# Kernel tuning notes

Measured on AMD Instinct MI355X. Metric: run time of the kernel, lower is better.

## Reference

```python
import jax, jax.numpy as jnp
import numpy as np

E, H, O = 300, 256, 2            # embedding_size, hidden_size, output_size
N_SENT, SENT_LEN, CLAIM_LEN = 2048, 64, 64


def setup_inputs() -> dict:
    key = jax.random.key(0)
    ks = jax.random.split(key, 24)
    rn = lambda k, shape, s=0.05: (jax.random.normal(k, shape, jnp.float32) * s)
    return {
        "claim": jax.random.normal(ks[0], (CLAIM_LEN, E), jnp.float32),
        "sentences": jax.random.normal(ks[1], (N_SENT, SENT_LEN, E), jnp.float32),
        # claim GRU (PyTorch layout: W_ih (3H,E), W_hh (3H,H), gates ordered r,z,n)
        "Wih_c": rn(ks[2], (3 * H, E)), "Whh_c": rn(ks[3], (3 * H, H)),
        "bih_c": rn(ks[4], (3 * H,)), "bhh_c": rn(ks[5], (3 * H,)),
        # sentence GRU
        "Wih_s": rn(ks[6], (3 * H, E)), "Whh_s": rn(ks[7], (3 * H, H)),
        "bih_s": rn(ks[8], (3 * H,)), "bhh_s": rn(ks[9], (3 * H,)),
        # gates (no bias)
        "Wg_s": rn(ks[10], (1, H)), "Wg_c": rn(ks[11], (1, H)),
        # coherence attention
        "Wac": rn(ks[12], (H, H)), "bac": rn(ks[13], (H,)),
        "Was": rn(ks[14], (1, H)), "bas": rn(ks[15], (1,)),
        # extension linear (H, 2H)
        "Wext": rn(ks[16], (H, 2 * H)), "bext": rn(ks[17], (H,)),
        # joint linear (H, 4H), no bias
        "Wj": rn(ks[18], (H, 4 * H)),
        # entailment attention
        "Wae": rn(ks[19], (1, H)), "bae": rn(ks[20], (1,)),
        # final classifier
        "Wf": rn(ks[21], (O, H)), "bf": rn(ks[22], (O,)),
    }


def _gru_last(x, Wih, Whh, bih, bhh):
    """x: (T, B, E) -> final hidden state (B, H). PyTorch GRU math, zero init."""
    B = x.shape[1]
    Hd = Whh.shape[1]
    gi = jnp.einsum('tbe,ge->tbg', x, Wih) + bih  # (T, B, 3H), input projections

    def step(h, gi_t):
        gh = h @ Whh.T + bhh
        ir, iz, inn = jnp.split(gi_t, 3, axis=-1)
        hr, hz, hn = jnp.split(gh, 3, axis=-1)
        r = jax.nn.sigmoid(ir + hr)
        z = jax.nn.sigmoid(iz + hz)
        n = jnp.tanh(inn + r * hn)
        return (1.0 - z) * n + z * h, None

    h0 = jnp.zeros((B, Hd), x.dtype)
    hT, _ = jax.lax.scan(step, h0, gi)
    return hT


def reference(claim, sentences, Wih_c, Whh_c, bih_c, bhh_c,
              Wih_s, Whh_s, bih_s, bhh_s, Wg_s, Wg_c,
              Wac, bac, Was, bas, Wext, bext, Wj, Wae, bae, Wf, bf):
    # claim encoder: (T,1,E) -> hc (1,H)
    hc = _gru_last(claim[:, None, :], Wih_c, Whh_c, bih_c, bhh_c)
    # batched sentence encoder (replaces the per-sentence Python loop)
    HS = _gru_last(jnp.transpose(sentences, (1, 0, 2)), Wih_s, Whh_s, bih_s, bhh_s)  # (N,H)
    # gated fusion of sentence reps with claim rep
    g = jax.nn.sigmoid(HS @ Wg_s.T + hc @ Wg_c.T)          # (N,1)
    HSg = g * HS + (1.0 - g) * hc                           # (N,H)
    # coherence attention over sentences (row-wise softmax)
    scores = (HSg @ Wac.T + bac) @ HSg.T + (HSg @ Was.T + bas)  # (N,N)
    coh = jax.nn.softmax(scores, axis=1)
    H_apo = coh @ HSg                                       # (N,H)
    H_tilde = jnp.tanh(jnp.concatenate([HS, H_apo], axis=1) @ Wext.T + bext)  # (N,H)
    # joint claim-sentence entailment features (replaces per-row loop)
    hc_b = jnp.broadcast_to(hc, H_tilde.shape)
    joint_in = jnp.concatenate(
        [hc_b, H_tilde, hc * H_tilde, jnp.abs(hc - H_tilde)], axis=1)  # (N,4H)
    H_c_s = jnp.tanh(joint_in @ Wj.T)                       # (N,H)
    # entailment attention (softmax over sentence axis)
    ae = jnp.tanh(H_c_s @ Wae.T + bae)                      # (N,1)
    w = jax.nn.softmax(ae, axis=0)                          # (N,1)
    h_c_S = w.T @ H_c_s                                     # (1,H)
    return jax.nn.sigmoid(h_c_S @ Wf.T + bf)                # (1,O)
```

## Files before the change

kernel.cpp:

```cpp
#include <hip/hip_runtime.h>

typedef unsigned short u16;
typedef unsigned int u32;
typedef short bf16x8 __attribute__((ext_vector_type(8)));
typedef float f32x4 __attribute__((ext_vector_type(4)));
typedef u16 u16x4v __attribute__((ext_vector_type(4)));

__device__ __forceinline__ float b2f(u16 h){ return __uint_as_float(((unsigned)h)<<16); }
__device__ __forceinline__ u16 f2b(float f){
  unsigned u = __float_as_uint(f);
  u += 0x7fffu + ((u>>16)&1u);
  return (u16)(u>>16);
}
__device__ __forceinline__ float sigm(float x){ return 1.f/(1.f+__expf(-x)); }
__device__ __forceinline__ float tanh_(float x){
  float ax=fabsf(x), e=__expf(-2.f*ax), t=(1.f-e)/(1.f+e);
  return x<0.f? -t : t;
}
__device__ __forceinline__ bf16x8 ld8a(const u16* p){
  union{ u16x4v h[2]; bf16x8 v; } u;
  u.h[0]=*(const u16x4v*)p; u.h[1]=*(const u16x4v*)(p+4); return u.v;
}
__device__ __forceinline__ f32x4 mfma16(bf16x8 a, bf16x8 b, f32x4 c){
  return __builtin_amdgcn_mfma_f32_16x16x32_bf16(a,b,c,0,0,0);
}

__global__ __launch_bounds__(256) void cvt_kernel(
    const float* __restrict__ WihS, const float* __restrict__ WhhS,
    const float* __restrict__ WihC, const float* __restrict__ WhhC,
    const float* __restrict__ Wac,  const float* __restrict__ Wext,
    const float* __restrict__ Wj,
    const float* __restrict__ bihS, const float* __restrict__ bhhS,
    const float* __restrict__ bihC, const float* __restrict__ bhhC,
    u16* __restrict__ WihP, u16* __restrict__ WhhSb,
    u16* __restrict__ WihCP, u16* __restrict__ WhhCb,
    u16* __restrict__ WacB, u16* __restrict__ WextB, u16* __restrict__ WjB,
    float* __restrict__ biasGI, float* __restrict__ biasGIC)
{
  const int seg = blockIdx.y;
  int n;
  switch(seg){
    case 0: n = 768*320; break;  case 1: n = 196608; break;
    case 2: n = 768*320; break;  case 3: n = 196608; break;
    case 4: n = 65536; break;    case 5: n = 131072; break;
    case 6: n = 262144; break;   default: n = 1536; break;
  }
  for (int i = blockIdx.x*256 + threadIdx.x; i < n; i += gridDim.x*256){
    switch(seg){
      case 0: { int r=i/320, c=i-r*320; WihP[i]  = (c<300)? f2b(WihS[r*300+c]) : (u16)0; } break;
      case 1: WhhSb[i] = f2b(WhhS[i]); break;
      case 2: { int r=i/320, c=i-r*320; WihCP[i] = (c<300)? f2b(WihC[r*300+c]) : (u16)0; } break;
      case 3: WhhCb[i] = f2b(WhhC[i]); break;
      case 4: WacB[i]  = f2b(Wac[i]);  break;
      case 5: WextB[i] = f2b(Wext[i]); break;
      case 6: WjB[i]   = f2b(Wj[i]);   break;
      default:
        if (i < 768) biasGI[i] = bihS[i] + (i < 512 ? bhhS[i] : 0.f);
        else { int j = i - 768; biasGIC[j] = bihC[j] + (j < 512 ? bhhC[j] : 0.f); }
        break;
    }
  }
}

__global__ __launch_bounds__(512) void gi_kernel(
    const int pass,
    const float* __restrict__ sents, const float* __restrict__ claim,
    const u16* __restrict__ WihP, const float* __restrict__ biasGI,
    const u16* __restrict__ WihCP, const float* __restrict__ biasGIC,
    u16* __restrict__ gi_b, float* __restrict__ giC)
{
  __shared__ __align__(16) u16 SA[64*320];
  const int tid=threadIdx.x, w=tid>>6, l=tid&63, ar=l&15, kg8=(l>>4)*8;
  const f32x4 z4 = {0.f,0.f,0.f,0.f};
  const bool isClaim = (blockIdx.x == 1024);
  const int b = blockIdx.x;

  for (int i=tid; i<64*80; i+=512){
    int r = i/80, q = i - r*80;
    u16x4v o;
    if (q < 75){
      float4 v;
      if (!isClaim) v = ((const float4*)sents)[(long)(2*b + (r>>5))*4800 + (pass*32 + (r&31))*75 + q];
      else          v = ((const float4*)claim)[r*75 + q];
      o[0]=f2b(v.x); o[1]=f2b(v.y); o[2]=f2b(v.z); o[3]=f2b(v.w);
    } else { o[0]=0; o[1]=0; o[2]=0; o[3]=0; }
    int byte = r*640 + q*8; byte ^= (r&7)<<4;
    *(u16x4v*)((char*)SA + byte) = o;
  }
  __syncthreads();

  const u16* Bw = isClaim ? WihCP : WihP;
  f32x4 acc[24];
  #pragma unroll
  for (int q=0;q<24;q++) acc[q]=z4;
  #pragma unroll
  for (int kc=0;kc<10;kc++){
    bf16x8 bq[6];
    #pragma unroll
    for (int q=0;q<6;q++) bq[q] = ld8a(Bw + (w*96 + q*16 + ar)*320 + kc*32 + kg8);
    #pragma unroll
    for (int m=0;m<4;m++){
      const int abyte = ((m*16+ar)*640 + (kc*32+kg8)*2) ^ ((ar&7)<<4);
      const bf16x8 a = *(const bf16x8*)((const char*)SA + abyte);
      #pragma unroll
      for (int q=0;q<6;q++) acc[m*6+q] = mfma16(a, bq[q], acc[m*6+q]);
    }
  }
  const int rb = (l>>4)*4;
  if (!isClaim){
    #pragma unroll
    for (int q=0;q<6;q++){
      const int c = w*96 + q*16 + ar;
      const float bs = biasGI[c];
      #pragma unroll
      for (int m=0;m<4;m++)
        #pragma unroll
        for (int p=0;p<4;p++)
          gi_b[(long)(b*64 + m*16 + rb + p)*768 + c] = f2b(acc[m*6+q][p] + bs);
    }
  } else {
    #pragma unroll
    for (int q=0;q<6;q++){
      const int c = w*96 + q*16 + ar;
      const float bs = biasGIC[c];
      #pragma unroll
      for (int m=0;m<4;m++)
        #pragma unroll
        for (int p=0;p<4;p++)
          giC[(m*16 + rb + p)*768 + c] = acc[m*6+q][p] + bs;
    }
  }
}

__global__ __attribute__((amdgpu_flat_work_group_size(512,512), amdgpu_waves_per_eu(2,2)))
void rec_kernel(
    const int pass,
    const u16* __restrict__ gi_b, const u16* __restrict__ WhhSb,
    const float* __restrict__ bhhS,
    float* __restrict__ Hmid, u16* __restrict__ HSout,
    const float* __restrict__ giC, const u16* __restrict__ WhhCb,
    const float* __restrict__ bhhC, const float* __restrict__ Wj,
    const float* __restrict__ WgC,
    float* __restrict__ hcMid, float* __restrict__ hcf,
    float* __restrict__ cvec, float* __restrict__ c0p)
{
  __shared__ __align__(16) u16 Hb[2][16][256];
  __shared__ __align__(16) u16 giL[2][8][776];
  __shared__ float ghL[768];
  __shared__ float hfL[256];
  __shared__ __align__(16) u16 hbL[256];
  const int tid=threadIdx.x, w=tid>>6, l=tid&63, ar=l&15, kg8=(l>>4)*8;
  const f32x4 z4 = {0.f,0.f,0.f,0.f};

  if (blockIdx.x < 256){
    const long i0 = (long)blockIdx.x*8;
    const int rb = (l>>4)*4;
    bf16x8 wf[6][8];
    #pragma unroll
    for (int s=0;s<3;s++)
      #pragma unroll
      for (int ti=0;ti<2;ti++)
        #pragma unroll
        for (int kc=0;kc<8;kc++)
          wf[s*2+ti][kc] = ld8a(WhhSb + (s*256 + w*32 + ti*16 + ar)*256 + kc*32 + kg8);
    const float bhn0 = bhhS[512 + w*32 +  0 + ar];
    const float bhn1 = bhhS[512 + w*32 + 16 + ar];

    for (int i=tid; i<2*16*256; i+=512) ((u16*)Hb)[i] = 0;
    __syncthreads();
    float hold[2][4];
    #pragma unroll
    for (int ti=0;ti<2;ti++)
      #pragma unroll
      for (int p=0;p<4;p++) hold[ti][p] = 0.f;
    if (pass==1 && l<32){
      #pragma unroll
      for (int ti=0;ti<2;ti++){
        #pragma unroll
        for (int p=0;p<4;p++){
          const int c = w*32 + ti*16 + ar, rr = rb + p;
          const float h = Hmid[(i0+rr)*256 + c];
          hold[ti][p] = h;
          const int byte = (rr*512 + c*2) ^ ((rr&7)<<4);
          *(u16*)((char*)&Hb[0][0][0] + byte) = f2b(h);
        }
      }
    }
    const u32* g32 = (const u32*)gi_b;
    u32 pf[6];
    #pragma unroll
    for (int rep=0;rep<6;rep++){
      const int i = rep*512 + tid, j = i/384, cu = i - j*384;
      pf[rep] = g32[((i0+j)*32 + 0)*384 + cu];
    }
    #pragma unroll
    for (int rep=0;rep<6;rep++){
      const int i = rep*512 + tid, j = i/384, cu = i - j*384;
      *(u32*)((char*)&giL[0][0][0] + j*1552 + cu*4) = pf[rep];
    }
    __syncthreads();

    int cur = 0;
    for (int tl=0; tl<32; tl++){
      const int tn = (tl<31) ? tl+1 : 31;
      #pragma unroll
      for (int rep=0;rep<6;rep++){
        const int i = rep*512 + tid, j = i/384, cu = i - j*384;
        pf[rep] = g32[((i0+j)*32 + tn)*384 + cu];
      }
      f32x4 acc[6];
      #pragma unroll
      for (int q=0;q<6;q++) acc[q]=z4;
      if (l < 32){
        #pragma unroll
        for (int s=0;s<2;s++)
          #pragma unroll
          for (int ti=0;ti<2;ti++)
            #pragma unroll
            for (int p=0;p<4;p++){
              const int c = w*32 + ti*16 + ar;
              const u16 v = *(const u16*)((const char*)&giL[cur][0][0] + (rb+p)*1552 + (s*256+c)*2);
              acc[s*2+ti][p] = b2f(v);
            }
      }
      #pragma unroll
      for (int kc=0;kc<8;kc++){
        const int abyte = (ar*512 + (kc*32+kg8)*2) ^ ((ar&7)<<4);
        const bf16x8 a = *(const bf16x8*)((const char*)&Hb[cur][0][0] + abyte);
        #pragma unroll
        for (int q=0;q<6;q++) acc[q] = mfma16(a, wf[q][kc], acc[q]);
      }
      #pragma unroll
      for (int rep=0;rep<6;rep++){
        const int i = rep*512 + tid, j = i/384, cu = i - j*384;
        *(u32*)((char*)&giL[cur^1][0][0] + j*1552 + cu*4) = pf[rep];
      }
      if (l < 32){
        #pragma unroll
        for (int ti=0;ti<2;ti++){
          const int c = w*32 + ti*16 + ar;
          const float bhn = ti ? bhn1 : bhn0;
          #pragma unroll
          for (int p=0;p<4;p++){
            const int rr = rb + p;
            const u16 gv = *(const u16*)((const char*)&giL[cur][0][0] + rr*1552 + (512+c)*2);
            const float r_ = sigm(acc[0+ti][p]);
            const float z_ = sigm(acc[2+ti][p]);
            const float n_ = tanh_(b2f(gv) + r_*(acc[4+ti][p] + bhn));
            const float h = (1.f - z_)*n_ + z_*hold[ti][p];
            hold[ti][p] = h;
            const int byte = (rr*512 + c*2) ^ ((rr&7)<<4);
            *(u16*)((char*)&Hb[cur^1][0][0] + byte) = f2b(h);
          }
        }
      }
      __syncthreads();
      cur ^= 1;
    }
    if (l < 32){
      #pragma unroll
      for (int ti=0;ti<2;ti++){
        #pragma unroll
        for (int p=0;p<4;p++){
          const int c = w*32 + ti*16 + ar, rr = rb + p;
          if (pass==0) Hmid[(i0+rr)*256 + c] = hold[ti][p];
          else         HSout[(i0+rr)*512 + c] = f2b(hold[ti][p]);
        }
      }
    }
  } else {
    const u16* wrow[6];
    #pragma unroll
    for (int q=0;q<6;q++) wrow[q] = WhhCb + (w*96 + q*16 + ar)*256 + kg8;
    if (tid < 256){
      const float h0 = (pass==0) ? 0.f : hcMid[tid];
      hfL[tid] = h0; hbL[tid] = f2b(h0);
    }
    __syncthreads();
    for (int tl=0; tl<32; tl++){
      const int t = pass*32 + tl;
      f32x4 a6[6];
      #pragma unroll
      for (int q=0;q<6;q++) a6[q]=z4;
      #pragma unroll
      for (int kc=0;kc<8;kc++){
        bf16x8 wq[6];
        #pragma unroll
        for (int q=0;q<6;q++) wq[q] = ld8a(wrow[q] + kc*32);
        const bf16x8 a = ld8a((const u16*)hbL + kc*32 + kg8);
        #pragma unroll
        for (int q=0;q<6;q++) a6[q] = mfma16(a, wq[q], a6[q]);
      }
      if (l < 16){
        #pragma unroll
        for (int q=0;q<6;q++) ghL[w*96 + q*16 + l] = a6[q][0];
      }
      __syncthreads();
      if (tid < 256){
        const int c = tid;
        const float r_ = sigm(giC[t*768 +       c] + ghL[c]);
        const float z_ = sigm(giC[t*768 + 256 + c] + ghL[256 + c]);
        const float n_ = tanh_(giC[t*768 + 512 + c] + r_*(ghL[512 + c] + bhhC[512 + c]));
        const float h = (1.f - z_)*n_ + z_*hfL[c];
        hfL[c] = h; hbL[c] = f2b(h);
      }
      __syncthreads();
    }
    if (tid < 256){
      const int c = tid;
      const float hv = hfL[c];
      if (pass == 0) hcMid[c] = hv;
      else {
        hcf[c] = hv;
        float acc2 = 0.f;
        for (int k=0;k<256;k++) acc2 += hfL[k]*Wj[(long)c*1024 + k];
        cvec[c] = acc2;
        if (c==0){ float s=0.f; for (int k=0;k<256;k++) s += hfL[k]*WgC[k]; *c0p = s; }
      }
    }
  }
}

__global__ __launch_bounds__(256) void fusion_kernel(
    const u16* __restrict__ HSH, const float* __restrict__ Wgs,
    const float* __restrict__ hcf, const float* __restrict__ c0p,
    u16* __restrict__ HSg, u16* __restrict__ HSgT)
{
  __shared__ float gbuf[64];
  __shared__ __align__(16) u16 tile[64][258];
  const int tid=threadIdx.x, w=tid>>6, l=tid&63;
  const long i0 = (long)blockIdx.x * 64;
  const float c0 = *c0p;
  for (int rr=0; rr<16; rr++){
    long i = i0 + w*16 + rr;
    float p = 0.f;
    for (int c=l; c<256; c+=64) p += b2f(HSH[i*512+c]) * Wgs[c];
    for (int o=32;o;o>>=1) p += __shfl_down(p,o,64);
    if (l==0) gbuf[w*16+rr] = sigm(p + c0);
  }
  __syncthreads();
  for (int idx=tid; idx<64*256; idx+=256){
    int r = idx>>8, c = idx&255;
    float g = gbuf[r];
    float hs = b2f(HSH[(i0+r)*512 + c]);
    u16 bv = f2b(g*hs + (1.f-g)*hcf[c]);
    HSg[(i0+r)*256 + c] = bv;
    tile[r][c] = bv;
  }
  __syncthreads();
  const int ioff = tid&63, cg = tid>>6;
  for (int cc=cg; cc<256; cc+=4)
    HSgT[(long)cc*2048 + i0 + ioff] = tile[ioff][cc];
}

template<int MODE>
__global__ __launch_bounds__(256) void gemmk(
    const u16* __restrict__ A, long lda,
    const u16* __restrict__ Bw, long ldb,
    void* __restrict__ Cp, long ldc, int K,
    const float* __restrict__ biasf,
    const float* __restrict__ hc)
{
  const int tid=threadIdx.x, w=tid>>6, l=tid&63, ar=l&15, kg8=(l>>4)*8;
  const long row0 = (long)blockIdx.x*64 + w*16;
  const long col0 = (long)blockIdx.y*64;
  const f32x4 z4 = {0.f,0.f,0.f,0.f};
  f32x4 acc[4] = {z4,z4,z4,z4};
  const u16* ap = A + (row0+ar)*lda + kg8;
  const u16* bp0 = Bw + (col0+ 0+ar)*ldb + kg8;
  const u16* bp1 = Bw + (col0+16+ar)*ldb + kg8;
  const u16* bp2 = Bw + (col0+32+ar)*ldb + kg8;
  const u16* bp3 = Bw + (col0+48+ar)*ldb + kg8;
  for (int k0=0; k0<K; k0+=32){
    bf16x8 a = ld8a(ap + k0);
    acc[0] = mfma16(a, ld8a(bp0+k0), acc[0]);
    acc[1] = mfma16(a, ld8a(bp1+k0), acc[1]);
    acc[2] = mfma16(a, ld8a(bp2+k0), acc[2]);
    acc[3] = mfma16(a, ld8a(bp3+k0), acc[3]);
  }
  const int rbase = (l>>4)*4;
  #pragma unroll
  for (int t=0;t<4;t++){
    long c = col0 + t*16 + ar;
    #pragma unroll
    for (int p=0;p<4;p++){
      long r = row0 + rbase + p;
      float v = acc[t][p];
      if constexpr (MODE==0){
        if (biasf) v += biasf[c];
        ((u16*)Cp)[r*ldc + c] = f2b(v);
      } else if constexpr (MODE==1){
        ((float*)Cp)[r*ldc + c] = v;
      } else if constexpr (MODE==2){
        float tv = tanh_(v + biasf[c]);
        u16* Uo = (u16*)Cp;
        float hv = hc[c];
        Uo[r*768 + c]       = f2b(tv);
        Uo[r*768 + 256 + c] = f2b(hv*tv);
        Uo[r*768 + 512 + c] = f2b(fabsf(hv - tv));
      } else {
        float tv = tanh_(v + biasf[c]);
        ((u16*)Cp)[r*ldc + c] = f2b(tv);
      }
    }
  }
}

__global__ __launch_bounds__(256) void softmax_rows(float* __restrict__ S)
{
  __shared__ float buf[2048];
  __shared__ float red[4];
  const long i = blockIdx.x;
  float* row = S + i*2048;
  const int tid = threadIdx.x;
  float m = -1e30f;
  for (int c=tid; c<2048; c+=256){ float v=row[c]; buf[c]=v; m=fmaxf(m,v); }
  for (int o=32;o;o>>=1) m = fmaxf(m, __shfl_down(m,o,64));
  if ((tid&63)==0) red[tid>>6] = m;
  __syncthreads();
  m = fmaxf(fmaxf(red[0],red[1]), fmaxf(red[2],red[3]));
  __syncthreads();
  float s = 0.f;
  for (int c=tid; c<2048; c+=256){ float e=__expf(buf[c]-m); buf[c]=e; s+=e; }
  for (int o=32;o;o>>=1) s += __shfl_down(s,o,64);
  if ((tid&63)==0) red[tid>>6] = s;
  __syncthreads();
  s = red[0]+red[1]+red[2]+red[3];
  const float rinv = 1.f/s;
  u16* P = (u16*)S + i*4096;
  for (int c=tid; c<2048; c+=256) P[c] = f2b(buf[c]*rinv);
}

__global__ __launch_bounds__(256) void ae_kernel(
    const u16* __restrict__ Hcs, const float* __restrict__ Wae, const float* __restrict__ bae,
    float* __restrict__ part, float* __restrict__ psum)
{
  __shared__ float aebuf[64];
  const int b=blockIdx.x, tid=threadIdx.x, w=tid>>6, l=tid&63;
  const long i0 = (long)b*64;
  const float baev = bae[0];
  for (int rr=0; rr<16; rr++){
    long i = i0 + w*16 + rr;
    float p = 0.f;
    for (int c=l; c<256; c+=64) p += b2f(Hcs[i*256+c]) * Wae[c];
    for (int o=32;o;o>>=1) p += __shfl_down(p,o,64);
    if (l==0) aebuf[w*16+rr] = __expf(tanh_(p + baev));
  }
  __syncthreads();
  float acc = 0.f;
  const int c = tid;
  for (int r=0;r<64;r++) acc += aebuf[r] * b2f(Hcs[(i0+r)*256 + c]);
  part[b*256 + c] = acc;
  if (tid==0){ float s=0.f; for (int r=0;r<64;r++) s+=aebuf[r]; psum[b]=s; }
}

__global__ __launch_bounds__(256) void final_kernel(
    const float* __restrict__ part, const float* __restrict__ psum,
    const float* __restrict__ Wf, const float* __restrict__ bf_, float* __restrict__ out)
{
  __shared__ float hbuf[256];
  __shared__ float ssum;
  const int tid = threadIdx.x;
  float v = 0.f;
  for (int b=0;b<32;b++) v += part[b*256 + tid];
  hbuf[tid] = v;
  if (tid==0){ float s=0.f; for (int b=0;b<32;b++) s+=psum[b]; ssum=s; }
  __syncthreads();
  const int w = tid>>6, l = tid&63;
  if (w < 2){
    float rinv = 1.f/ssum;
    float p = 0.f;
    for (int c=l; c<256; c+=64) p += hbuf[c]*rinv*Wf[w*256 + c];
    for (int o=32;o;o>>=1) p += __shfl_down(p,o,64);
    if (l==0) out[w] = sigm(p + bf_[w]);
  }
}

extern "C" void kernel_launch(void* const* d_in, const int* in_sizes, int n_in,
                              void* d_out, int out_size, void* d_ws, size_t ws_size,
                              hipStream_t stream)
{
  const float* claim=(const float*)d_in[0];
  const float* sents=(const float*)d_in[1];
  const float* WihC =(const float*)d_in[2];
  const float* WhhC =(const float*)d_in[3];
  const float* bihC =(const float*)d_in[4];
  const float* bhhC =(const float*)d_in[5];
  const float* WihS =(const float*)d_in[6];
  const float* WhhS =(const float*)d_in[7];
  const float* bihS =(const float*)d_in[8];
  const float* bhhS =(const float*)d_in[9];
  const float* WgS  =(const float*)d_in[10];
  const float* WgC  =(const float*)d_in[11];
  const float* Wac  =(const float*)d_in[12];
  const float* bac  =(const float*)d_in[13];
  const float* Wext =(const float*)d_in[16];
  const float* bext =(const float*)d_in[17];
  const float* Wj   =(const float*)d_in[18];
  const float* Wae  =(const float*)d_in[19];
  const float* bae  =(const float*)d_in[20];
  const float* Wf   =(const float*)d_in[21];
  const float* bf_  =(const float*)d_in[22];

  char* ws = (char*)d_ws;
  size_t off = 0;
  auto alloc = [&](size_t b)->void*{ void* p = ws + off; off = (off + b + 255) & ~(size_t)255; return p; };
  float* hcf  = (float*)alloc(256*4);
  float* cvec = (float*)alloc(256*4);
  float* c0p  = (float*)alloc(16);
  float* hcMid= (float*)alloc(256*4);
  float* giC  = (float*)alloc((size_t)64*768*4);
  u16* WihP   = (u16*)alloc((size_t)768*320*2);
  u16* WhhSb  = (u16*)alloc((size_t)196608*2);
  u16* WihCP  = (u16*)alloc((size_t)768*320*2);
  u16* WhhCb  = (u16*)alloc((size_t)196608*2);
  u16* WacB   = (u16*)alloc((size_t)65536*2);
  u16* WextB  = (u16*)alloc((size_t)131072*2);
  u16* WjB    = (u16*)alloc((size_t)262144*2);
  float* biasGI  = (float*)alloc(768*4);
  float* biasGIC = (float*)alloc(768*4);
  u16* HSH  = (u16*)alloc((size_t)2048*512*2);
  u16* HSg  = (u16*)alloc((size_t)2048*256*2);
  u16* HSgT = (u16*)alloc((size_t)256*2048*2);
  u16* A1   = (u16*)alloc((size_t)2048*256*2);
  u16* Up   = (u16*)alloc((size_t)2048*768*2);
  u16* Hcs  = (u16*)alloc((size_t)2048*256*2);
  float* part = (float*)alloc(32*256*4);
  float* psum = (float*)alloc(32*4);
  float* Hmid = (float*)alloc((size_t)2048*256*4);
  u16* gi_b   = (u16*)alloc((size_t)65536*768*2);
  float* S    = (float*)gi_b;

  cvt_kernel<<<dim3(960,8),256,0,stream>>>(WihS,WhhS,WihC,WhhC,Wac,Wext,Wj,
                                           bihS,bhhS,bihC,bhhC,
                                           WihP,WhhSb,WihCP,WhhCb,WacB,WextB,WjB,
                                           biasGI,biasGIC);
  gi_kernel<<<1025,512,0,stream>>>(0,sents,claim,WihP,biasGI,WihCP,biasGIC,gi_b,giC);
  rec_kernel<<<257,512,0,stream>>>(0,gi_b,WhhSb,bhhS,Hmid,HSH,
                                   giC,WhhCb,bhhC,Wj,WgC,hcMid,hcf,cvec,c0p);
  gi_kernel<<<1024,512,0,stream>>>(1,sents,claim,WihP,biasGI,WihCP,biasGIC,gi_b,giC);
  rec_kernel<<<257,512,0,stream>>>(1,gi_b,WhhSb,bhhS,Hmid,HSH,
                                   giC,WhhCb,bhhC,Wj,WgC,hcMid,hcf,cvec,c0p);

  fusion_kernel<<<32,256,0,stream>>>(HSH,WgS,hcf,c0p,HSg,HSgT);
  gemmk<0><<<dim3(32,4),256,0,stream>>>(HSg,256L,WacB,256L,(void*)A1,256L,256,bac,nullptr);
  gemmk<1><<<dim3(32,32),256,0,stream>>>(A1,256L,HSg,256L,(void*)S,2048L,256,nullptr,nullptr);
  softmax_rows<<<2048,256,0,stream>>>(S);
  gemmk<0><<<dim3(32,4),256,0,stream>>>((const u16*)S,4096L,HSgT,2048L,(void*)(HSH+256),512L,2048,nullptr,nullptr);
  gemmk<2><<<dim3(32,4),256,0,stream>>>(HSH,512L,WextB,512L,(void*)Up,768L,512,bext,hcf);
  gemmk<3><<<dim3(32,4),256,0,stream>>>(Up,768L,WjB+256,1024L,(void*)Hcs,256L,768,cvec,nullptr);
  ae_kernel<<<32,256,0,stream>>>(Hcs,Wae,bae,part,psum);
  final_kernel<<<1,256,0,stream>>>(part,psum,Wf,bf_,(float*)d_out);
}
```

Measured before the change: 827.5 us.

## Double rec_kernel workgroup to 16 waves and double-buffer gi B-fragment loads

The sentence GRU recurrence kernel now runs 1024 threads per block, so each wave owns 16 hidden columns instead of 32. This halves the MFMA count and register-held Whh fragments per wave along the serial time chain, and the gi prefetch is respread across the extra waves. The claim-GRU branch maps the extra waves onto the existing 8-wave work and only lets the first 8 write. Separately, gi_kernel prefetches the next k-chunk of weight fragments while issuing MFMAs on the current one, in exchange for more registers and the chance that the larger block lowers occupancy.

```diff
diff --git a/kernel.cpp b/kernel.cpp
--- a/kernel.cpp
+++ b/kernel.cpp
@@ -90,20 +90,39 @@
   __syncthreads();
 
   const u16* Bw = isClaim ? WihCP : WihP;
+  const u16* brow[6];
+  #pragma unroll
+  for (int q=0;q<6;q++) brow[q] = Bw + (w*96 + q*16 + ar)*320 + kg8;
+
   f32x4 acc[24];
   #pragma unroll
   for (int q=0;q<24;q++) acc[q]=z4;
+
+  bf16x8 bq0[6], bq1[6];
   #pragma unroll
-  for (int kc=0;kc<10;kc++){
-    bf16x8 bq[6];
-    #pragma unroll
-    for (int q=0;q<6;q++) bq[q] = ld8a(Bw + (w*96 + q*16 + ar)*320 + kc*32 + kg8);
+  for (int q=0;q<6;q++) bq0[q] = ld8a(brow[q]);
+  #pragma unroll
+  for (int kp=0;kp<5;kp++){
+    const int k0 = 2*kp, k1 = 2*kp+1;
+    #pragma unroll
+    for (int q=0;q<6;q++) bq1[q] = ld8a(brow[q] + k1*32);
     #pragma unroll
     for (int m=0;m<4;m++){
-      const int abyte = ((m*16+ar)*640 + (kc*32+kg8)*2) ^ ((ar&7)<<4);
+      const int abyte = ((m*16+ar)*640 + (k0*32+kg8)*2) ^ ((ar&7)<<4);
       const bf16x8 a = *(const bf16x8*)((const char*)SA + abyte);
       #pragma unroll
-      for (int q=0;q<6;q++) acc[m*6+q] = mfma16(a, bq[q], acc[m*6+q]);
+      for (int q=0;q<6;q++) acc[m*6+q] = mfma16(a, bq0[q], acc[m*6+q]);
+    }
+    if (kp < 4){
+      #pragma unroll
+      for (int q=0;q<6;q++) bq0[q] = ld8a(brow[q] + (k1+1)*32);
+    }
+    #pragma unroll
+    for (int m=0;m<4;m++){
+      const int abyte = ((m*16+ar)*640 + (k1*32+kg8)*2) ^ ((ar&7)<<4);
+      const bf16x8 a = *(const bf16x8*)((const char*)SA + abyte);
+      #pragma unroll
+      for (int q=0;q<6;q++) acc[m*6+q] = mfma16(a, bq1[q], acc[m*6+q]);
     }
   }
   const int rb = (l>>4)*4;
@@ -132,8 +151,7 @@
   }
 }
 
-__global__ __attribute__((amdgpu_flat_work_group_size(512,512), amdgpu_waves_per_eu(2,2)))
-void rec_kernel(
+__global__ __launch_bounds__(1024) void rec_kernel(
     const int pass,
     const u16* __restrict__ gi_b, const u16* __restrict__ WhhSb,
     const float* __restrict__ bhhS,
@@ -155,123 +173,105 @@
   if (blockIdx.x < 256){
     const long i0 = (long)blockIdx.x*8;
     const int rb = (l>>4)*4;
-    bf16x8 wf[6][8];
+    bf16x8 wf[3][8];
     #pragma unroll
     for (int s=0;s<3;s++)
       #pragma unroll
-      for (int ti=0;ti<2;ti++)
-        #pragma unroll
-        for (int kc=0;kc<8;kc++)
-          wf[s*2+ti][kc] = ld8a(WhhSb + (s*256 + w*32 + ti*16 + ar)*256 + kc*32 + kg8);
-    const float bhn0 = bhhS[512 + w*32 +  0 + ar];
-    const float bhn1 = bhhS[512 + w*32 + 16 + ar];
-
-    for (int i=tid; i<2*16*256; i+=512) ((u16*)Hb)[i] = 0;
+      for (int kc=0;kc<8;kc++)
+        wf[s][kc] = ld8a(WhhSb + (s*256 + w*16 + ar)*256 + kc*32 + kg8);
+    const float bhn = bhhS[512 + w*16 + ar];
+
+    const u32* g0 = (const u32*)gi_b;
+    int ldsoff[3], gidx[3];
+    #pragma unroll
+    for (int r=0;r<3;r++){
+      const int task = w + r*16;
+      const int j = task/6, seg = task - j*6;
+      ldsoff[r] = j*1552 + seg*256 + l*4;
+      gidx[r]   = (int)(((i0+j)*32)*384) + seg*64 + l;
+    }
+
+    for (int i=tid; i<2*16*256; i+=1024) ((u16*)Hb)[i] = 0;
     __syncthreads();
-    float hold[2][4];
-    #pragma unroll
-    for (int ti=0;ti<2;ti++)
-      #pragma unroll
-      for (int p=0;p<4;p++) hold[ti][p] = 0.f;
+    float hold[4];
+    #pragma unroll
+    for (int p=0;p<4;p++) hold[p] = 0.f;
+    const int cb2 = (w*16 + ar)*2;
     if (pass==1 && l<32){
-      #pragma unroll
-      for (int ti=0;ti<2;ti++){
-        #pragma unroll
-        for (int p=0;p<4;p++){
-          const int c = w*32 + ti*16 + ar, rr = rb + p;
-          const float h = Hmid[(i0+rr)*256 + c];
-          hold[ti][p] = h;
-          const int byte = (rr*512 + c*2) ^ ((rr&7)<<4);
-          *(u16*)((char*)&Hb[0][0][0] + byte) = f2b(h);
-        }
-      }
-    }
-    const u32* g32 = (const u32*)gi_b;
-    u32 pf[6];
-    #pragma unroll
-    for (int rep=0;rep<6;rep++){
-      const int i = rep*512 + tid, j = i/384, cu = i - j*384;
-      pf[rep] = g32[((i0+j)*32 + 0)*384 + cu];
-    }
-    #pragma unroll
-    for (int rep=0;rep<6;rep++){
-      const int i = rep*512 + tid, j = i/384, cu = i - j*384;
-      *(u32*)((char*)&giL[0][0][0] + j*1552 + cu*4) = pf[rep];
-    }
+      const int c = w*16 + ar;
+      #pragma unroll
+      for (int p=0;p<4;p++){
+        const int rr = rb + p;
+        const float h = Hmid[(i0+rr)*256 + c];
+        hold[p] = h;
+        const int byte = (rr*512 + c*2) ^ ((rr&7)<<4);
+        *(u16*)((char*)&Hb[0][0][0] + byte) = f2b(h);
+      }
+    }
+    u32 pf[3];
+    #pragma unroll
+    for (int r=0;r<3;r++) pf[r] = g0[gidx[r]];
+    #pragma unroll
+    for (int r=0;r<3;r++) *(u32*)((char*)&giL[0][0][0] + ldsoff[r]) = pf[r];
     __syncthreads();
 
     int cur = 0;
     for (int tl=0; tl<32; tl++){
       const int tn = (tl<31) ? tl+1 : 31;
       #pragma unroll
-      for (int rep=0;rep<6;rep++){
-        const int i = rep*512 + tid, j = i/384, cu = i - j*384;
-        pf[rep] = g32[((i0+j)*32 + tn)*384 + cu];
-      }
-      f32x4 acc[6];
-      #pragma unroll
-      for (int q=0;q<6;q++) acc[q]=z4;
+      for (int r=0;r<3;r++) pf[r] = g0[gidx[r] + tn*384];
+      f32x4 acc[3];
+      acc[0]=z4; acc[1]=z4; acc[2]=z4;
       if (l < 32){
         #pragma unroll
         for (int s=0;s<2;s++)
           #pragma unroll
-          for (int ti=0;ti<2;ti++)
-            #pragma unroll
-            for (int p=0;p<4;p++){
-              const int c = w*32 + ti*16 + ar;
-              const u16 v = *(const u16*)((const char*)&giL[cur][0][0] + (rb+p)*1552 + (s*256+c)*2);
-              acc[s*2+ti][p] = b2f(v);
-            }
+          for (int p=0;p<4;p++){
+            const u16 v = *(const u16*)((const char*)&giL[cur][0][0] + (rb+p)*1552 + s*512 + cb2);
+            acc[s][p] = b2f(v);
+          }
       }
       #pragma unroll
       for (int kc=0;kc<8;kc++){
         const int abyte = (ar*512 + (kc*32+kg8)*2) ^ ((ar&7)<<4);
         const bf16x8 a = *(const bf16x8*)((const char*)&Hb[cur][0][0] + abyte);
-        #pragma unroll
-        for (int q=0;q<6;q++) acc[q] = mfma16(a, wf[q][kc], acc[q]);
-      }
-      #pragma unroll
-      for (int rep=0;rep<6;rep++){
-        const int i = rep*512 + tid, j = i/384, cu = i - j*384;
-        *(u32*)((char*)&giL[cur^1][0][0] + j*1552 + cu*4) = pf[rep];
-      }
+        acc[0] = mfma16(a, wf[0][kc], acc[0]);
+        acc[1] = mfma16(a, wf[1][kc], acc[1]);
+        acc[2] = mfma16(a, wf[2][kc], acc[2]);
+      }
+      #pragma unroll
+      for (int r=0;r<3;r++) *(u32*)((char*)&giL[cur^1][0][0] + ldsoff[r]) = pf[r];
       if (l < 32){
         #pragma unroll
-        for (int ti=0;ti<2;ti++){
-          const int c = w*32 + ti*16 + ar;
-          const float bhn = ti ? bhn1 : bhn0;
-          #pragma unroll
-          for (int p=0;p<4;p++){
-            const int rr = rb + p;
-            const u16 gv = *(const u16*)((const char*)&giL[cur][0][0] + rr*1552 + (512+c)*2);
-            const float r_ = sigm(acc[0+ti][p]);
-            const float z_ = sigm(acc[2+ti][p]);
-            const float n_ = tanh_(b2f(gv) + r_*(acc[4+ti][p] + bhn));
-            const float h = (1.f - z_)*n_ + z_*hold[ti][p];
-            hold[ti][p] = h;
-            const int byte = (rr*512 + c*2) ^ ((rr&7)<<4);
-            *(u16*)((char*)&Hb[cur^1][0][0] + byte) = f2b(h);
-          }
+        for (int p=0;p<4;p++){
+          const int rr = rb + p;
+          const u16 gv = *(const u16*)((const char*)&giL[cur][0][0] + rr*1552 + 1024 + cb2);
+          const float r_ = sigm(acc[0][p]);
+          const float z_ = sigm(acc[1][p]);
+          const float n_ = tanh_(b2f(gv) + r_*(acc[2][p] + bhn));
+          const float h = (1.f - z_)*n_ + z_*hold[p];
+          hold[p] = h;
+          const int byte = (rr*512 + cb2) ^ ((rr&7)<<4);
+          *(u16*)((char*)&Hb[cur^1][0][0] + byte) = f2b(h);
         }
       }
       __syncthreads();
       cur ^= 1;
     }
     if (l < 32){
-      #pragma unroll
-      for (int ti=0;ti<2;ti++){
-        #pragma unroll
-        for (int p=0;p<4;p++){
-          const int c = w*32 + ti*16 + ar, rr = rb + p;
-          if (pass==0) Hmid[(i0+rr)*256 + c] = hold[ti][p];
-          else         HSout[(i0+rr)*512 + c] = f2b(hold[ti][p]);
-        }
+      const int c = w*16 + ar;
+      #pragma unroll
+      for (int p=0;p<4;p++){
+        const int rr = rb + p;
+        if (pass==0) Hmid[(i0+rr)*256 + c] = hold[p];
+        else         HSout[(i0+rr)*512 + c] = f2b(hold[p]);
       }
     }
   } else {
+    const int wc = w & 7;
     const u16* wrow[6];
     #pragma unroll
-    for (int q=0;q<6;q++) wrow[q] = WhhCb + (w*96 + q*16 + ar)*256 + kg8;
+    for (int q=0;q<6;q++) wrow[q] = WhhCb + (wc*96 + q*16 + ar)*256 + kg8;
     if (tid < 256){
       const float h0 = (pass==0) ? 0.f : hcMid[tid];
       hfL[tid] = h0; hbL[tid] = f2b(h0);
@@ -291,9 +291,9 @@
         #pragma unroll
         for (int q=0;q<6;q++) a6[q] = mfma16(a, wq[q], a6[q]);
       }
-      if (l < 16){
-        #pragma unroll
-        for (int q=0;q<6;q++) ghL[w*96 + q*16 + l] = a6[q][0];
+      if (l < 16 && w < 8){
+        #pragma unroll
+        for (int q=0;q<6;q++) ghL[wc*96 + q*16 + l] = a6[q][0];
       }
       __syncthreads();
       if (tid < 256){
@@ -536,11 +536,11 @@
                                            WihP,WhhSb,WihCP,WhhCb,WacB,WextB,WjB,
                                            biasGI,biasGIC);
   gi_kernel<<<1025,512,0,stream>>>(0,sents,claim,WihP,biasGI,WihCP,biasGIC,gi_b,giC);
-  rec_kernel<<<257,512,0,stream>>>(0,gi_b,WhhSb,bhhS,Hmid,HSH,
-                                   giC,WhhCb,bhhC,Wj,WgC,hcMid,hcf,cvec,c0p);
+  rec_kernel<<<257,1024,0,stream>>>(0,gi_b,WhhSb,bhhS,Hmid,HSH,
+                                    giC,WhhCb,bhhC,Wj,WgC,hcMid,hcf,cvec,c0p);
   gi_kernel<<<1024,512,0,stream>>>(1,sents,claim,WihP,biasGI,WihCP,biasGIC,gi_b,giC);
-  rec_kernel<<<257,512,0,stream>>>(1,gi_b,WhhSb,bhhS,Hmid,HSH,
-                                   giC,WhhCb,bhhC,Wj,WgC,hcMid,hcf,cvec,c0p);
+  rec_kernel<<<257,1024,0,stream>>>(1,gi_b,WhhSb,bhhS,Hmid,HSH,
+                                    giC,WhhCb,bhhC,Wj,WgC,hcMid,hcf,cvec,c0p);
 
   fusion_kernel<<<32,256,0,stream>>>(HSH,WgS,hcf,c0p,HSg,HSgT);
   gemmk<0><<<dim3(32,4),256,0,stream>>>(HSg,256L,WacB,256L,(void*)A1,256L,256,bac,nullptr);
```

Measured after the change: 1.592 ms. +92.3%, slower.

## Double-buffer weight loads in input-projection GEMM and reorder recurrence block roles

Applied to the files above, without the earlier changes.

The input-projection GEMM loop now double-buffers the B-operand global loads, prefetching the next k-chunk's weight fragments while MFMAs run on the current one. This is meant to hide global load latency behind compute, at the cost of doubled register usage for the B fragments. The recurrence kernel drops its explicit waves_per_eu(2,2) hint in favour of plain launch_bounds and adds an asm clobber of v250, which raises the VGPR allocation. It also moves the claim-path block from the last block index to block 0, so the sentence blocks start at index 1. These changes alter register allocation and occupancy and may change scheduling order. The visible part of the diff does not show whether the claim branch was updated to match the new block index.

```diff
diff --git a/kernel.cpp b/kernel.cpp
--- a/kernel.cpp
+++ b/kernel.cpp
@@ -90,20 +90,39 @@
   __syncthreads();
 
   const u16* Bw = isClaim ? WihCP : WihP;
+  const u16* brow[6];
+  #pragma unroll
+  for (int q=0;q<6;q++) brow[q] = Bw + (w*96 + q*16 + ar)*320 + kg8;
+
   f32x4 acc[24];
   #pragma unroll
   for (int q=0;q<24;q++) acc[q]=z4;
+
+  bf16x8 bq0[6], bq1[6];
   #pragma unroll
-  for (int kc=0;kc<10;kc++){
-    bf16x8 bq[6];
-    #pragma unroll
-    for (int q=0;q<6;q++) bq[q] = ld8a(Bw + (w*96 + q*16 + ar)*320 + kc*32 + kg8);
+  for (int q=0;q<6;q++) bq0[q] = ld8a(brow[q]);
+  #pragma unroll
+  for (int kp=0;kp<5;kp++){
+    const int k0 = 2*kp, k1 = 2*kp+1;
+    #pragma unroll
+    for (int q=0;q<6;q++) bq1[q] = ld8a(brow[q] + k1*32);
     #pragma unroll
     for (int m=0;m<4;m++){
-      const int abyte = ((m*16+ar)*640 + (kc*32+kg8)*2) ^ ((ar&7)<<4);
+      const int abyte = ((m*16+ar)*640 + (k0*32+kg8)*2) ^ ((ar&7)<<4);
       const bf16x8 a = *(const bf16x8*)((const char*)SA + abyte);
       #pragma unroll
-      for (int q=0;q<6;q++) acc[m*6+q] = mfma16(a, bq[q], acc[m*6+q]);
+      for (int q=0;q<6;q++) acc[m*6+q] = mfma16(a, bq0[q], acc[m*6+q]);
+    }
+    if (kp < 4){
+      #pragma unroll
+      for (int q=0;q<6;q++) bq0[q] = ld8a(brow[q] + (k1+1)*32);
+    }
+    #pragma unroll
+    for (int m=0;m<4;m++){
+      const int abyte = ((m*16+ar)*640 + (k1*32+kg8)*2) ^ ((ar&7)<<4);
+      const bf16x8 a = *(const bf16x8*)((const char*)SA + abyte);
+      #pragma unroll
+      for (int q=0;q<6;q++) acc[m*6+q] = mfma16(a, bq1[q], acc[m*6+q]);
     }
   }
   const int rb = (l>>4)*4;
@@ -132,8 +151,7 @@
   }
 }
 
-__global__ __attribute__((amdgpu_flat_work_group_size(512,512), amdgpu_waves_per_eu(2,2)))
-void rec_kernel(
+__global__ __launch_bounds__(512) void rec_kernel(
     const int pass,
     const u16* __restrict__ gi_b, const u16* __restrict__ WhhSb,
     const float* __restrict__ bhhS,
@@ -152,8 +170,10 @@
   const int tid=threadIdx.x, w=tid>>6, l=tid&63, ar=l&15, kg8=(l>>4)*8;
   const f32x4 z4 = {0.f,0.f,0.f,0.f};
 
-  if (blockIdx.x < 256){
-    const long i0 = (long)blockIdx.x*8;
+  asm volatile("" ::: "v250");
+
+  if (blockIdx.x != 0){
+    const long i0 = (long)(blockIdx.x - 1)*8;
     const int rb = (l>>4)*4;
     bf16x8 wf[6][8];
     #pragma unroll
```

New measurement: 815.5 us. No clear change (-1.4%).

## Stream GRU weights through double-buffered LDS via direct global-to-LDS loads

Applied to the files above, without the earlier changes.

The input-projection kernel now stages each K-slice of the W_ih weights into a double-buffered LDS tile using global_load_lds, with a swizzled layout, instead of loading B fragments straight from global memory. The recurrent kernel stops holding the whole W_hh slice in registers. It re-streams W_hh from global into double-buffered LDS for every K-chunk of every timestep, and also swaps the claim block to index 0 and drops the waves-per-EU hint. This is meant to relieve register pressure and hide weight-load latency. The cost is much more LDS traffic, a barrier per K-chunk inside the serial recurrence, and repeated L2 reads of the weights on the latency-critical path.

```diff
diff --git a/kernel.cpp b/kernel.cpp
--- a/kernel.cpp
+++ b/kernel.cpp
@@ -23,6 +23,27 @@
 }
 __device__ __forceinline__ f32x4 mfma16(bf16x8 a, bf16x8 b, f32x4 c){
   return __builtin_amdgcn_mfma_f32_16x16x32_bf16(a,b,c,0,0,0);
+}
+
+__device__ __forceinline__ void gl_lds16(const void* g, void* s){
+  __builtin_amdgcn_global_load_lds(
+      (const __attribute__((address_space(1))) void*)g,
+      (__attribute__((address_space(3))) void*)s, 16, 0, 0);
+}
+
+__device__ __forceinline__ void stage_rows(const u16* base, int ld, int kc,
+                                           u16* buf, int w, int l){
+  #pragma unroll
+  for (int ii=0; ii<6; ii++){
+    const int i   = w + ii*8;
+    const int row = i*16 + (l>>2);
+    const int c8  = (l&3) ^ ((row>>2)&3);
+    gl_lds16(base + (long)row*ld + kc*32 + c8*8, buf + i*512);
+  }
+}
+__device__ __forceinline__ bf16x8 ldB(const u16* buf, int row, int l){
+  const int slot = (l>>4) ^ ((row>>2)&3);
+  return *(const bf16x8*)((const char*)buf + row*64 + slot*16);
 }
 
 __global__ __launch_bounds__(256) void cvt_kernel(
@@ -70,6 +91,7 @@
     u16* __restrict__ gi_b, float* __restrict__ giC)
 {
   __shared__ __align__(16) u16 SA[64*320];
+  __shared__ __align__(16) u16 BB[2][768*32];
   const int tid=threadIdx.x, w=tid>>6, l=tid&63, ar=l&15, kg8=(l>>4)*8;
   const f32x4 z4 = {0.f,0.f,0.f,0.f};
   const bool isClaim = (blockIdx.x == 1024);
@@ -87,17 +109,21 @@
     int byte = r*640 + q*8; byte ^= (r&7)<<4;
     *(u16x4v*)((char*)SA + byte) = o;
   }
-  __syncthreads();
-
   const u16* Bw = isClaim ? WihCP : WihP;
+  stage_rows(Bw, 320, 0, BB[0], w, l);
+  __syncthreads();
+
   f32x4 acc[24];
   #pragma unroll
   for (int q=0;q<24;q++) acc[q]=z4;
+
+  int cur = 0;
   #pragma unroll
   for (int kc=0;kc<10;kc++){
+    if (kc < 9) stage_rows(Bw, 320, kc+1, BB[cur^1], w, l);
     bf16x8 bq[6];
     #pragma unroll
-    for (int q=0;q<6;q++) bq[q] = ld8a(Bw + (w*96 + q*16 + ar)*320 + kc*32 + kg8);
+    for (int q=0;q<6;q++) bq[q] = ldB(BB[cur], w*96 + q*16 + ar, l);
     #pragma unroll
     for (int m=0;m<4;m++){
       const int abyte = ((m*16+ar)*640 + (kc*32+kg8)*2) ^ ((ar&7)<<4);
@@ -105,6 +131,8 @@
       #pragma unroll
       for (int q=0;q<6;q++) acc[m*6+q] = mfma16(a, bq[q], acc[m*6+q]);
     }
+    __syncthreads();
+    cur ^= 1;
   }
   const int rb = (l>>4)*4;
   if (!isClaim){
@@ -132,8 +160,7 @@
   }
 }
 
-__global__ __attribute__((amdgpu_flat_work_group_size(512,512), amdgpu_waves_per_eu(2,2)))
-void rec_kernel(
+__global__ __launch_bounds__(512) void rec_kernel(
     const int pass,
     const u16* __restrict__ gi_b, const u16* __restrict__ WhhSb,
     const float* __restrict__ bhhS,
@@ -146,23 +173,16 @@
 {
   __shared__ __align__(16) u16 Hb[2][16][256];
   __shared__ __align__(16) u16 giL[2][8][776];
+  __shared__ __align__(16) u16 WB[2][768*32];
   __shared__ float ghL[768];
   __shared__ float hfL[256];
   __shared__ __align__(16) u16 hbL[256];
   const int tid=threadIdx.x, w=tid>>6, l=tid&63, ar=l&15, kg8=(l>>4)*8;
   const f32x4 z4 = {0.f,0.f,0.f,0.f};
 
-  if (blockIdx.x < 256){
-    const long i0 = (long)blockIdx.x*8;
+  if (blockIdx.x != 0){
+    const long i0 = (long)(blockIdx.x - 1)*8;
     const int rb = (l>>4)*4;
-    bf16x8 wf[6][8];
-    #pragma unroll
-    for (int s=0;s<3;s++)
-      #pragma unroll
-      for (int ti=0;ti<2;ti++)
-        #pragma unroll
-        for (int kc=0;kc<8;kc++)
-          wf[s*2+ti][kc] = ld8a(WhhSb + (s*256 + w*32 + ti*16 + ar)*256 + kc*32 + kg8);
     const float bhn0 = bhhS[512 + w*32 +  0 + ar];
     const float bhn1 = bhhS[512 + w*32 + 16 + ar];
 
@@ -198,9 +218,10 @@
       const int i = rep*512 + tid, j = i/384, cu = i - j*384;
       *(u32*)((char*)&giL[0][0][0] + j*1552 + cu*4) = pf[rep];
     }
+    stage_rows(WhhSb, 256, 0, WB[0], w, l);
     __syncthreads();
 
-    int cur = 0;
+    int cur = 0, kb = 0;
     for (int tl=0; tl<32; tl++){
       const int tn = (tl<31) ? tl+1 : 31;
       #pragma unroll
@@ -225,10 +246,20 @@
       }
       #pragma unroll
       for (int kc=0;kc<8;kc++){
+        const int nkc = (kc<7) ? kc+1 : 0;
+        stage_rows(WhhSb, 256, nkc, WB[kb^1], w, l);
         const int abyte = (ar*512 + (kc*32+kg8)*2) ^ ((ar&7)<<4);
         const bf16x8 a = *(const bf16x8*)((const char*)&Hb[cur][0][0] + abyte);
-        #pragma unroll
-        for (int q=0;q<6;q++) acc[q] = mfma16(a, wf[q][kc], acc[q]);
+        bf16x8 wq[6];
+        #pragma unroll
+        for (int s=0;s<3;s++)
+          #pragma unroll
+          for (int ti=0;ti<2;ti++)
+            wq[s*2+ti] = ldB(WB[kb], s*256 + w*32 + ti*16 + ar, l);
+        #pragma unroll
+        for (int q=0;q<6;q++) acc[q] = mfma16(a, wq[q], acc[q]);
+        __syncthreads();
+        kb ^= 1;
       }
       #pragma unroll
       for (int rep=0;rep<6;rep++){
```

Measured after the change: 960.0 us. 1.16x slower.
